# Kernel tuning notes

Hardware: AMD Instinct MI355X
Metric: run time of the kernel (lower is better)

The kernel has to match this reference:

```python
import jax, jax.numpy as jnp
import numpy as np

N_HEAD = 16


def setup_inputs() -> dict:
    key = jax.random.key(0)
    ks = jax.random.split(key, 6)
    B, T, C = 2, 2048, 1024
    hs = C // N_HEAD  # 64
    block_minus_1 = 2048  # block_size - 1
    x = jax.random.normal(ks[0], (B, T, C), dtype=jnp.float32)
    W1 = jax.random.normal(ks[1], (C, C), dtype=jnp.float32) * (1.0 / np.sqrt(C))
    b1 = jnp.zeros((C,), dtype=jnp.float32)
    # original init: uniform(-1e-3, 1e-3)
    w2 = jax.random.uniform(ks[2], (hs, block_minus_1), dtype=jnp.float32, minval=-1e-3, maxval=1e-3)
    b2 = jnp.zeros((block_minus_1,), dtype=jnp.float32)
    Wv = jax.random.normal(ks[3], (C, C), dtype=jnp.float32) * (1.0 / np.sqrt(C))
    bv = jnp.zeros((C,), dtype=jnp.float32)
    Wp = jax.random.normal(ks[4], (C, C), dtype=jnp.float32) * (1.0 / np.sqrt(C))
    bp = jnp.zeros((C,), dtype=jnp.float32)
    return {"x": x, "W1": W1, "b1": b1, "w2": w2, "b2": b2,
            "Wv": Wv, "bv": bv, "Wp": Wp, "bp": bp}


def reference(x, W1, b1, w2, b2, Wv, bv, Wp, bp):
    B, T, C = x.shape
    hs = C // N_HEAD
    r = jax.nn.relu(x @ W1.T + b1).reshape(B, T, N_HEAD, hs).transpose(0, 2, 1, 3)
    # synthesizer scores: (B, nh, T, T) = relu_out @ w2[:, :T] + b2[:T]
    att = jnp.einsum('bhtd,dj->bhtj', r, w2[:, :T]) + b2[:T]
    causal = jnp.tril(jnp.ones((T, T), dtype=bool))
    att = jnp.where(causal[None, None], att, jnp.float32(-1e10))
    att = jax.nn.softmax(att, axis=-1)  # attn_drop = 0 (eval)
    v = (x @ Wv.T + bv).reshape(B, T, N_HEAD, hs).transpose(0, 2, 1, 3)
    y = jnp.einsum('bhtj,bhjd->bhtd', att, v)
    y = y.transpose(0, 2, 1, 3).reshape(B, T, C)
    return y @ Wp.T + bp  # resid_drop = 0 (eval)
```

## Files before the change

kernel.cpp:

```cpp
#include <hip/hip_runtime.h>

typedef __bf16 bf16x8 __attribute__((ext_vector_type(8)));
typedef float f32x4 __attribute__((ext_vector_type(4)));

__device__ __forceinline__ unsigned short f2bf(float f) {
  union { float f; unsigned u; } v; v.f = f;
  unsigned u = v.u;
  return (unsigned short)((u + 0x7fffu + ((u >> 16) & 1u)) >> 16);
}
__device__ __forceinline__ unsigned short f2bf_fast(float f) {
  union { float f; unsigned u; } v; v.f = f;
  return (unsigned short)((v.u + 0x8000u) >> 16);
}
__device__ __forceinline__ void gload_lds16(const void* g, void* l) {
  __builtin_amdgcn_global_load_lds(
      (const __attribute__((address_space(1))) unsigned int*)g,
      (__attribute__((address_space(3))) unsigned int*)l, 16, 0, 0);
}
__device__ __forceinline__ void cvt4(const float* __restrict__ s,
                                     unsigned short* __restrict__ d, int u) {
  f32x4 v = ((const f32x4*)s)[u];
  union { unsigned short s[4]; unsigned long long u; } o;
  o.s[0] = f2bf(v[0]); o.s[1] = f2bf(v[1]); o.s[2] = f2bf(v[2]); o.s[3] = f2bf(v[3]);
  ((unsigned long long*)d)[u] = o.u;
}


__global__ void prep(const float* __restrict__ x, const float* __restrict__ W1,
                     const float* __restrict__ Wv, const float* __restrict__ Wp,
                     const float* __restrict__ w2, const float* __restrict__ b2,
                     unsigned short* __restrict__ xb, unsigned short* __restrict__ W1b,
                     unsigned short* __restrict__ Wvb, unsigned short* __restrict__ Wpb,
                     unsigned short* __restrict__ w2t, unsigned short* __restrict__ ebj) {
  int u = blockIdx.x * 256 + threadIdx.x;
  if (u < 1048576) { cvt4(x, xb, u); return; }
  u -= 1048576;
  if (u < 262144) { cvt4(W1, W1b, u); return; }
  u -= 262144;
  if (u < 262144) { cvt4(Wv, Wvb, u); return; }
  u -= 262144;
  if (u < 262144) { cvt4(Wp, Wpb, u); return; }
  u -= 262144;
  if (u < 32768) {
    int j = u >> 4, d4 = (u & 15) * 4;
    union { unsigned short s[4]; unsigned long long x; } o;
#pragma unroll
    for (int i = 0; i < 4; ++i) o.s[i] = f2bf(w2[(d4 + i) * 2048 + j]);
    ((unsigned long long*)w2t)[u] = o.x;
    return;
  }
  u -= 32768;
  union { unsigned short s[4]; unsigned long long x; } o;
#pragma unroll
  for (int i = 0; i < 4; ++i) o.s[i] = f2bf(__expf(b2[u * 4 + i]));
  ((unsigned long long*)ebj)[u] = o.x;
}

__global__ __launch_bounds__(256) void gemm_rv(
    const unsigned short* __restrict__ xb, const unsigned short* __restrict__ W1b,
    const unsigned short* __restrict__ Wvb, const float* __restrict__ b1,
    const float* __restrict__ bv, const float* __restrict__ b2,
    unsigned short* __restrict__ rb, unsigned short* __restrict__ vtb) {
  __shared__ unsigned short As[128 * 64];
  __shared__ unsigned short Bs[64 * 64];
  int id = blockIdx.x;
  const unsigned short *A, *Bt;
  const float* bias;
  unsigned short* C;
  int N, tileM, tileN, epi;
  if (id < 512) {
    A = xb; Bt = W1b; bias = b1; C = rb; N = 1024; epi = 0;
    tileN = (id & 15) * 64; tileM = (id >> 4) * 128;
  } else {
    id -= 512;
    A = Wvb; Bt = xb; bias = bv; C = vtb; N = 4096; epi = 1;
    tileN = (id & 63) * 64; tileM = (id >> 6) * 128;
  }
  const int tid = threadIdx.x;
  const int wv = tid >> 6, ln = tid & 63;
  const int quad = ln >> 4, lq = ln & 15;
  const int rowL = ln >> 3;
  const int kc = (((ln & 7) ^ rowL) & 7) * 8;
  const int sx = lq & 7;
  const int ko0 = (quad ^ sx) * 8, ko1 = ((4 + quad) ^ sx) * 8;

  f32x4 acc[2][4];
  const f32x4 zf = {0.f, 0.f, 0.f, 0.f};
#pragma unroll
  for (int i = 0; i < 2; ++i)
#pragma unroll
    for (int j = 0; j < 4; ++j) acc[i][j] = zf;

  for (int k0 = 0; k0 < 1024; k0 += 64) {
    __syncthreads();
#pragma unroll
    for (int l = 0; l < 4; ++l) {
      int row = l * 32 + wv * 8 + rowL;
      gload_lds16(A + (tileM + row) * 1024 + k0 + kc, &As[l * 2048 + wv * 512]);
    }
#pragma unroll
    for (int l = 0; l < 2; ++l) {
      int row = l * 32 + wv * 8 + rowL;
      gload_lds16(Bt + (tileN + row) * 1024 + k0 + kc, &Bs[l * 2048 + wv * 512]);
    }
    __syncthreads();
#pragma unroll
    for (int kk = 0; kk < 2; ++kk) {
      const int ko = kk ? ko1 : ko0;
      bf16x8 af[2], bfr[4];
#pragma unroll
      for (int mi = 0; mi < 2; ++mi)
        af[mi] = *(const bf16x8*)&As[(wv * 32 + mi * 16 + lq) * 64 + ko];
#pragma unroll
      for (int ni = 0; ni < 4; ++ni)
        bfr[ni] = *(const bf16x8*)&Bs[(ni * 16 + lq) * 64 + ko];
#pragma unroll
      for (int mi = 0; mi < 2; ++mi)
#pragma unroll
        for (int ni = 0; ni < 4; ++ni)
          acc[mi][ni] = __builtin_amdgcn_mfma_f32_16x16x32_bf16(af[mi], bfr[ni], acc[mi][ni], 0, 0, 0);
    }
  }
#pragma unroll
  for (int ni = 0; ni < 4; ++ni) {
    int col = tileN + ni * 16 + lq;
    float eb = (epi == 1) ? __expf(b2[col & 2047]) : 0.0f;
#pragma unroll
    for (int mi = 0; mi < 2; ++mi) {
#pragma unroll
      for (int rg = 0; rg < 4; ++rg) {
        int row = tileM + wv * 32 + mi * 16 + quad * 4 + rg;
        float v = acc[mi][ni][rg];
        if (epi == 0) {
          v += bias[col];
          v = v > 0.f ? v : 0.f;
        } else {
          v = (v + bias[row]) * eb;
        }
        C[row * N + col] = f2bf(v);
      }
    }
  }
}

__global__ __launch_bounds__(256) void gemm_p(
    const unsigned short* __restrict__ A, const unsigned short* __restrict__ Bt,
    const float* __restrict__ bias, float* __restrict__ C) {
  __shared__ unsigned short As[64 * 64];
  __shared__ unsigned short Bs[64 * 64];
  const int tid = threadIdx.x;
  const int wv = tid >> 6, ln = tid & 63;
  const int quad = ln >> 4, lq = ln & 15;
  const int tileM = blockIdx.y * 64, tileN = blockIdx.x * 64;
  const int rowL = ln >> 3;
  const int kc = (((ln & 7) ^ rowL) & 7) * 8;
  const int sx = lq & 7;
  const int ko0 = (quad ^ sx) * 8, ko1 = ((4 + quad) ^ sx) * 8;

  f32x4 acc[4];
  const f32x4 zf = {0.f, 0.f, 0.f, 0.f};
#pragma unroll
  for (int j = 0; j < 4; ++j) acc[j] = zf;

  for (int k0 = 0; k0 < 1024; k0 += 64) {
    __syncthreads();
#pragma unroll
    for (int l = 0; l < 2; ++l) {
      int row = l * 32 + wv * 8 + rowL;
      gload_lds16(A + (tileM + row) * 1024 + k0 + kc, &As[l * 2048 + wv * 512]);
      gload_lds16(Bt + (tileN + row) * 1024 + k0 + kc, &Bs[l * 2048 + wv * 512]);
    }
    __syncthreads();
#pragma unroll
    for (int kk = 0; kk < 2; ++kk) {
      const int ko = kk ? ko1 : ko0;
      bf16x8 af = *(const bf16x8*)&As[(wv * 16 + lq) * 64 + ko];
#pragma unroll
      for (int ni = 0; ni < 4; ++ni) {
        bf16x8 bfr = *(const bf16x8*)&Bs[(ni * 16 + lq) * 64 + ko];
        acc[ni] = __builtin_amdgcn_mfma_f32_16x16x32_bf16(af, bfr, acc[ni], 0, 0, 0);
      }
    }
  }
#pragma unroll
  for (int ni = 0; ni < 4; ++ni) {
    int col = tileN + ni * 16 + lq;
#pragma unroll
    for (int rg = 0; rg < 4; ++rg) {
      int row = tileM + wv * 16 + quad * 4 + rg;
      C[row * 1024 + col] = acc[ni][rg] + bias[col];
    }
  }
}

__global__ __launch_bounds__(256, 4) void attn(
    const unsigned short* __restrict__ r, const unsigned short* __restrict__ w2t,
    const unsigned short* __restrict__ vt, const unsigned short* __restrict__ ebj,
    unsigned short* __restrict__ y) {
  __shared__ unsigned short W2s[2][64 * 64];
  __shared__ unsigned short Vs[2][64 * 64];
  __shared__ unsigned short Ps[4][16 * 64];

  const int tid = threadIdx.x;
  const int wv = tid >> 6, ln = tid & 63;
  const int quad = ln >> 4, lq = ln & 15;
  const int bh = blockIdx.y, b = bh >> 4, h = bh & 15;
  const int tt = (31 - blockIdx.x + blockIdx.y) & 31;
  const int rowL = ln >> 3;
  const int kc = (((ln & 7) ^ rowL) & 7) * 8;
  const int sx = lq & 7;
  const int ko0 = (quad ^ sx) * 8, ko1 = ((4 + quad) ^ sx) * 8;
  const int t0 = tt * 64;

  bf16x8 ra0, ra1;
  {
    const unsigned short* base = r + (b * 2048 + t0 + wv * 16 + lq) * 1024 + h * 64 + quad * 8;
    ra0 = *(const bf16x8*)(base);
    ra1 = *(const bf16x8*)(base + 32);
  }

  f32x4 accY[4];
  f32x4 accL;
  const f32x4 zf = {0.f, 0.f, 0.f, 0.f};
#pragma unroll
  for (int nd = 0; nd < 4; ++nd) accY[nd] = zf;
  accL = zf;

  auto stage = [&](int jt, int bi) {
    int j0 = jt * 64;
#pragma unroll
    for (int l = 0; l < 2; ++l) {
      int row = l * 32 + wv * 8 + rowL;
      gload_lds16(w2t + (j0 + row) * 64 + kc, &W2s[bi][l * 2048 + wv * 512]);
      gload_lds16(vt + (h * 64 + row) * 4096 + b * 2048 + j0 + kc,
                  &Vs[bi][l * 2048 + wv * 512]);
    }
  };

  stage(0, 0);
  for (int jt = 0; jt <= tt; ++jt) {
    const int cb = jt & 1;
    __syncthreads();
    if (jt < tt) stage(jt + 1, cb ^ 1);
    const int j0 = jt * 64;

    bf16x8 eb0 = *(const bf16x8*)&ebj[j0 + quad * 8];
    bf16x8 eb1 = *(const bf16x8*)&ebj[j0 + 32 + quad * 8];
    bf16x8 w2f0[4], w2f1[4];
#pragma unroll
    for (int ni = 0; ni < 4; ++ni) {
      w2f0[ni] = *(const bf16x8*)&W2s[cb][(ni * 16 + lq) * 64 + ko0];
      w2f1[ni] = *(const bf16x8*)&W2s[cb][(ni * 16 + lq) * 64 + ko1];
    }

    f32x4 sv[4] = {zf, zf, zf, zf};
#pragma unroll
    for (int ni = 0; ni < 4; ++ni) {
      sv[ni] = __builtin_amdgcn_mfma_f32_16x16x32_bf16(ra0, w2f0[ni], sv[ni], 0, 0, 0);
      sv[ni] = __builtin_amdgcn_mfma_f32_16x16x32_bf16(ra1, w2f1[ni], sv[ni], 0, 0, 0);
    }

    const bool diag = (jt == tt);
#pragma unroll
    for (int ni = 0; ni < 4; ++ni) {
      int j = j0 + ni * 16 + lq;
#pragma unroll
      for (int rg = 0; rg < 4; ++rg) {
        float p = __expf(sv[ni][rg]);
        if (diag) {
          int t = t0 + wv * 16 + quad * 4 + rg;
          p = (j <= t) ? p : 0.f;
        }
        Ps[wv][(quad * 4 + rg) * 64 +
               (((ni * 2 + (lq >> 3)) ^ ((quad * 4 + rg) & 7)) * 8) + (lq & 7)] = f2bf_fast(p);
      }
    }

#pragma unroll
    for (int kk = 0; kk < 2; ++kk) {
      const int ko = kk ? ko1 : ko0;
      bf16x8 pa = *(const bf16x8*)&Ps[wv][lq * 64 + ko];
#pragma unroll
      for (int nd = 0; nd < 4; ++nd) {
        bf16x8 bb = *(const bf16x8*)&Vs[cb][(nd * 16 + lq) * 64 + ko];
        accY[nd] = __builtin_amdgcn_mfma_f32_16x16x32_bf16(pa, bb, accY[nd], 0, 0, 0);
      }
      accL = __builtin_amdgcn_mfma_f32_16x16x32_bf16(pa, kk ? eb1 : eb0, accL, 0, 0, 0);
    }
  }

  float inv[4];
#pragma unroll
  for (int rg = 0; rg < 4; ++rg) inv[rg] = __builtin_amdgcn_rcpf(accL[rg]);
#pragma unroll
  for (int nd = 0; nd < 4; ++nd)
#pragma unroll
    for (int rg = 0; rg < 4; ++rg) {
      int t = t0 + wv * 16 + quad * 4 + rg;
      y[(b * 2048 + t) * 1024 + h * 64 + nd * 16 + lq] = f2bf(accY[nd][rg] * inv[rg]);
    }
}

extern "C" void kernel_launch(void* const* d_in, const int* in_sizes, int n_in,
                              void* d_out, int out_size, void* d_ws, size_t ws_size,
                              hipStream_t stream) {
  const float* x  = (const float*)d_in[0];
  const float* W1 = (const float*)d_in[1];
  const float* b1 = (const float*)d_in[2];
  const float* w2 = (const float*)d_in[3];
  const float* b2 = (const float*)d_in[4];
  const float* Wv = (const float*)d_in[5];
  const float* bv = (const float*)d_in[6];
  const float* Wp = (const float*)d_in[7];
  const float* bp = (const float*)d_in[8];

  unsigned short* ws  = (unsigned short*)d_ws;
  unsigned short* xb   = ws;
  unsigned short* W1b  = ws + 4194304;
  unsigned short* Wvb  = ws + 5242880;
  unsigned short* Wpb  = ws + 6291456;
  unsigned short* w2t  = ws + 7340032;
  unsigned short* rb   = ws + 7471104;
  unsigned short* vt   = ws + 11665408;
  unsigned short* yb   = ws + 15859712;
  unsigned short* ebjb = ws + 20054016;

  prep<<<7298, 256, 0, stream>>>(x, W1, Wv, Wp, w2, b2, xb, W1b, Wvb, Wpb, w2t, ebjb);
  gemm_rv<<<1024, 256, 0, stream>>>(xb, W1b, Wvb, b1, bv, b2, rb, vt);
  attn<<<dim3(32, 32), 256, 0, stream>>>(rb, w2t, vt, ebjb, yb);
  gemm_p<<<dim3(16, 64), 256, 0, stream>>>(yb, Wpb, bp, (float*)d_out);
}
```

Baseline: 186.3 us.

## Pair complementary causal query tiles per attention block for balanced work

Each attention block now handles two query tiles, p and 31-p, running them one after the other in a single 33-iteration loop. Every block therefore does the same amount of causal work, which removes the triangular load imbalance across the grid. The grid is halved to 512 blocks and launch_bounds occupancy drops from 4 to 2, since extra registers hold two sets of query fragments. The cost is less parallelism and fewer waves per CU to hide latency.

```diff
diff --git a/kernel.cpp b/kernel.cpp
--- a/kernel.cpp
+++ b/kernel.cpp
@@ -193,7 +193,7 @@
   }
 }
 
-__global__ __launch_bounds__(256, 4) void attn(
+__global__ __launch_bounds__(256, 2) void attn(
     const unsigned short* __restrict__ r, const unsigned short* __restrict__ w2t,
     const unsigned short* __restrict__ vt, const unsigned short* __restrict__ ebj,
     unsigned short* __restrict__ y) {
@@ -204,19 +204,22 @@
   const int tid = threadIdx.x;
   const int wv = tid >> 6, ln = tid & 63;
   const int quad = ln >> 4, lq = ln & 15;
+  const int p = blockIdx.x;
   const int bh = blockIdx.y, b = bh >> 4, h = bh & 15;
-  const int tt = (31 - blockIdx.x + blockIdx.y) & 31;
+  const int ta = p, tb = 31 - p;
+  const int t0a = ta * 64, t0b = tb * 64;
   const int rowL = ln >> 3;
   const int kc = (((ln & 7) ^ rowL) & 7) * 8;
   const int sx = lq & 7;
   const int ko0 = (quad ^ sx) * 8, ko1 = ((4 + quad) ^ sx) * 8;
-  const int t0 = tt * 64;
-
-  bf16x8 ra0, ra1;
+
+  bf16x8 ra[2][2];
   {
-    const unsigned short* base = r + (b * 2048 + t0 + wv * 16 + lq) * 1024 + h * 64 + quad * 8;
-    ra0 = *(const bf16x8*)(base);
-    ra1 = *(const bf16x8*)(base + 32);
+    const unsigned short* base = r + (b * 2048 + wv * 16 + lq) * 1024 + h * 64 + quad * 8;
+    ra[0][0] = *(const bf16x8*)(base + t0a * 1024);
+    ra[0][1] = *(const bf16x8*)(base + t0a * 1024 + 32);
+    ra[1][0] = *(const bf16x8*)(base + t0b * 1024);
+    ra[1][1] = *(const bf16x8*)(base + t0b * 1024 + 32);
   }
 
   f32x4 accY[4];
@@ -238,10 +241,18 @@
   };
 
   stage(0, 0);
-  for (int jt = 0; jt <= tt; ++jt) {
-    const int cb = jt & 1;
-    __syncthreads();
-    if (jt < tt) stage(jt + 1, cb ^ 1);
+  for (int it = 0; it <= 32; ++it) {
+    const int cb = it & 1;
+    __syncthreads();
+    if (it < 32) {
+      int nit = it + 1;
+      int njt = (nit <= p) ? nit : (nit - p - 1);
+      stage(njt, cb ^ 1);
+    }
+    const int s = (it <= p) ? 0 : 1;
+    const int jt = (it <= p) ? it : (it - p - 1);
+    const int tts = s ? tb : ta;
+    const int t0 = tts * 64;
     const int j0 = jt * 64;
 
     bf16x8 eb0 = *(const bf16x8*)&ebj[j0 + quad * 8];
@@ -256,23 +267,23 @@
     f32x4 sv[4] = {zf, zf, zf, zf};
 #pragma unroll
     for (int ni = 0; ni < 4; ++ni) {
-      sv[ni] = __builtin_amdgcn_mfma_f32_16x16x32_bf16(ra0, w2f0[ni], sv[ni], 0, 0, 0);
-      sv[ni] = __builtin_amdgcn_mfma_f32_16x16x32_bf16(ra1, w2f1[ni], sv[ni], 0, 0, 0);
-    }
-
-    const bool diag = (jt == tt);
+      sv[ni] = __builtin_amdgcn_mfma_f32_16x16x32_bf16(ra[s][0], w2f0[ni], sv[ni], 0, 0, 0);
+      sv[ni] = __builtin_amdgcn_mfma_f32_16x16x32_bf16(ra[s][1], w2f1[ni], sv[ni], 0, 0, 0);
+    }
+
+    const bool diag = (jt == tts);
 #pragma unroll
     for (int ni = 0; ni < 4; ++ni) {
       int j = j0 + ni * 16 + lq;
 #pragma unroll
       for (int rg = 0; rg < 4; ++rg) {
-        float p = __expf(sv[ni][rg]);
+        float pe = __expf(sv[ni][rg]);
         if (diag) {
           int t = t0 + wv * 16 + quad * 4 + rg;
-          p = (j <= t) ? p : 0.f;
+          pe = (j <= t) ? pe : 0.f;
         }
         Ps[wv][(quad * 4 + rg) * 64 +
-               (((ni * 2 + (lq >> 3)) ^ ((quad * 4 + rg) & 7)) * 8) + (lq & 7)] = f2bf_fast(p);
+               (((ni * 2 + (lq >> 3)) ^ ((quad * 4 + rg) & 7)) * 8) + (lq & 7)] = f2bf_fast(pe);
       }
     }
 
@@ -287,18 +298,23 @@
       }
       accL = __builtin_amdgcn_mfma_f32_16x16x32_bf16(pa, kk ? eb1 : eb0, accL, 0, 0, 0);
     }
-  }
-
-  float inv[4];
-#pragma unroll
-  for (int rg = 0; rg < 4; ++rg) inv[rg] = __builtin_amdgcn_rcpf(accL[rg]);
-#pragma unroll
-  for (int nd = 0; nd < 4; ++nd)
-#pragma unroll
-    for (int rg = 0; rg < 4; ++rg) {
-      int t = t0 + wv * 16 + quad * 4 + rg;
-      y[(b * 2048 + t) * 1024 + h * 64 + nd * 16 + lq] = f2bf(accY[nd][rg] * inv[rg]);
-    }
+
+    if (it == p || it == 32) {
+      float inv[4];
+#pragma unroll
+      for (int rg = 0; rg < 4; ++rg) inv[rg] = __builtin_amdgcn_rcpf(accL[rg]);
+#pragma unroll
+      for (int nd = 0; nd < 4; ++nd)
+#pragma unroll
+        for (int rg = 0; rg < 4; ++rg) {
+          int t = t0 + wv * 16 + quad * 4 + rg;
+          y[(b * 2048 + t) * 1024 + h * 64 + nd * 16 + lq] = f2bf(accY[nd][rg] * inv[rg]);
+        }
+#pragma unroll
+      for (int nd = 0; nd < 4; ++nd) accY[nd] = zf;
+      accL = zf;
+    }
+  }
 }
 
 extern "C" void kernel_launch(void* const* d_in, const int* in_sizes, int n_in,
@@ -327,6 +343,6 @@
 
   prep<<<7298, 256, 0, stream>>>(x, W1, Wv, Wp, w2, b2, xb, W1b, Wvb, Wpb, w2t, ebjb);
   gemm_rv<<<1024, 256, 0, stream>>>(xb, W1b, Wvb, b1, bv, b2, rb, vt);
-  attn<<<dim3(32, 32), 256, 0, stream>>>(rb, w2t, vt, ebjb, yb);
+  attn<<<dim3(16, 32), 256, 0, stream>>>(rb, w2t, vt, ebjb, yb);
   gemm_p<<<dim3(16, 64), 256, 0, stream>>>(yb, Wpb, bp, (float*)d_out);
 }
```

Result: no change. 188.7 us (+1.3%).
